# Kernel tuning notes

Measured on AMD Instinct MI355X. Metric: run time of the kernel, lower is better.

Reference implementation:

```python
import jax, jax.numpy as jnp
import numpy as np

NEG_FILL = -10000.0  # matches masked_fill_(mask, -10000.0)


def setup_inputs() -> dict:
    key0 = jax.random.key(0)
    kq, kk, kv, km = jax.random.split(key0, 4)
    B, H, S, D = 2, 16, 2048, 64
    query = jax.random.normal(kq, (B, H, S, D), dtype=jnp.float32)
    key = jax.random.normal(kk, (B, H, S, D), dtype=jnp.float32)
    value = jax.random.normal(kv, (B, H, S, D), dtype=jnp.float32)
    # key-padding mask [B, S]; True = position is masked out
    mask = jax.random.randint(km, (B, S), 0, 2).astype(jnp.bool_)
    return {"query": query, "key": key, "value": value, "mask": mask}


def reference(query, key, value, mask):
    # scaled dot-product attention: [B,H,S,D] x [B,H,S,D] -> [B,H,S,S]
    scale = 1.0 / jnp.sqrt(jnp.asarray(query.shape[-1], query.dtype))
    scores = jnp.einsum('bhqd,bhkd->bhqk', query, key) * scale
    # mask [B,S] -> broadcast over heads and query positions as [B,1,1,S]
    scores = jnp.where(mask[:, None, None, :], jnp.asarray(NEG_FILL, scores.dtype), scores)
    attn = jax.nn.softmax(scores, axis=-1)
    # dropout probs are 0 (eval-mode identity)
    out = jnp.einsum('bhqk,bhkd->bhqd', attn, value)
    return out
```

## Files before the change

### kernel.cpp

```cpp
#include <hip/hip_runtime.h>
#include <hip/hip_bf16.h>
#include <stdint.h>

namespace {

constexpr int Bb = 2;
constexpr int Hh = 16;
constexpr int Ss = 2048;
constexpr int Dd = 64;
constexpr int KT = 64;
constexpr int NT = Ss / KT;
constexpr int TILE_BYTES = KT * Dd * 2;
constexpr int BH_BYTES = NT * TILE_BYTES;
constexpr size_t KPRE_BYTES = (size_t)Bb * Hh * Ss * Dd * 2;
constexpr size_t VPRE_OFF = KPRE_BYTES;
constexpr size_t MASK_OFF = 2 * KPRE_BYTES;
constexpr size_t WS_NEED = MASK_OFF + (size_t)Bb * NT * 8;

typedef __bf16 bf16x8 __attribute__((ext_vector_type(8)));
typedef float floatx4 __attribute__((ext_vector_type(4)));
typedef short short4v __attribute__((ext_vector_type(4)));
typedef short short8v __attribute__((ext_vector_type(8)));

typedef __attribute__((address_space(1))) const unsigned int guint;
typedef __attribute__((address_space(3))) unsigned int luint;

__device__ __forceinline__ void g2lds16(const void* g, void* l) {
  __builtin_amdgcn_global_load_lds((guint*)g, (luint*)l, 16, 0, 0);
}

__device__ __forceinline__ floatx4 mfma16(short4v a, short4v b, floatx4 c) {
#if __has_builtin(__builtin_amdgcn_mfma_f32_16x16x16bf16_1k)
  return __builtin_amdgcn_mfma_f32_16x16x16bf16_1k(a, b, c, 0, 0, 0);
#else
  floatx4 d;
  __asm__("v_mfma_f32_16x16x16_bf16 %0, %1, %2, %3" : "=v"(d) : "v"(a), "v"(b), "v"(c));
  return d;
#endif
}

__device__ __forceinline__ short bf2s(float x) {
  __bf16 h = (__bf16)x;
  return __builtin_bit_cast(short, h);
}

__global__ __launch_bounds__(256) void preprocess(
    const float* __restrict__ K, const float* __restrict__ V,
    const int* __restrict__ mask, uint8_t* __restrict__ ws)
{
  const int t = blockIdx.x * 256 + threadIdx.x;
  if (t < 524288) {
    const int c = t & 7, key = (t >> 3) & 2047, bh = t >> 14;
    const int row = key & 63, tile = key >> 6;
    const float4* src = (const float4*)(K + ((size_t)bh * 2048 + key) * 64 + c * 8);
    const float4 a = src[0], b = src[1];
    bf16x8 pk;
    pk[0] = (__bf16)a.x; pk[1] = (__bf16)a.y; pk[2] = (__bf16)a.z; pk[3] = (__bf16)a.w;
    pk[4] = (__bf16)b.x; pk[5] = (__bf16)b.y; pk[6] = (__bf16)b.z; pk[7] = (__bf16)b.w;
    uint8_t* dst = ws + (size_t)bh * BH_BYTES + tile * TILE_BYTES + row * 128 + ((c ^ (row & 7)) << 4);
    *(bf16x8*)dst = pk;
  } else if (t < 1048576) {
    const int v = t - 524288;
    const int c16 = v & 7, d = (v >> 3) & 63, kt = (v >> 9) & 31, bh = v >> 14;
    const int s2 = c16 & 1, q = c16 >> 1;
    const int kb = kt * 64 + 32 * s2 + q * 4;
    const float* src = V + ((size_t)bh * 2048 + kb) * 64 + d;
    bf16x8 pv;
#pragma unroll
    for (int i = 0; i < 4; ++i) pv[i] = (__bf16)src[i * 64];
#pragma unroll
    for (int i = 0; i < 4; ++i) pv[4 + i] = (__bf16)src[(16 + i) * 64];
    uint8_t* dst = ws + VPRE_OFF + (size_t)bh * BH_BYTES + kt * TILE_BYTES + d * 128 + ((c16 ^ (d & 7)) << 4);
    *(bf16x8*)dst = pv;
  } else if (t < 1048576 + 4096) {
    const int i = t - 1048576;
    const int bb = i >> 11, key = i & 2047;
    const unsigned long long bal = __ballot(mask[bb * 2048 + key] != 0);
    if ((key & 63) == 0)
      ((unsigned long long*)(ws + MASK_OFF))[bb * NT + (key >> 6)] = bal;
  }
}

#define NEGM (-14426.950408889634f)

__global__ __launch_bounds__(256, 2) void attn_fused3(
    const float* __restrict__ Q, const uint8_t* __restrict__ ws,
    float* __restrict__ Out)
{
  const int tid  = threadIdx.x;
  const int wave = tid >> 6;
  const int lane = tid & 63;
  const int ln   = lane & 15;
  const int quad = lane >> 4;

  const int bh   = blockIdx.x;
  const int qblk = blockIdx.y;
  const int b    = bh >> 4;

  const float* Qb = Q + (size_t)bh * Ss * Dd;
  float*       Ob = Out + (size_t)bh * Ss * Dd;
  const uint8_t* Kpre = ws + (size_t)bh * BH_BYTES;
  const uint8_t* Vpre = ws + VPRE_OFF + (size_t)bh * BH_BYTES;
  const unsigned long long* Mbits = (const unsigned long long*)(ws + MASK_OFF) + b * NT;

  __shared__ __align__(16) __bf16 Klds[2][KT * Dd];
  __shared__ __align__(16) __bf16 Vlds[2][KT * Dd];

  const int q0A = qblk * 128 + wave * 32;
  const int q0B = q0A + 16;

  const float QS = 0.125f * 1.44269504088896340736f;
  bf16x8 aqA0, aqA1, aqB0, aqB1;
  {
    const float* qpA = Qb + (size_t)(q0A + ln) * Dd + quad * 8;
    const float* qpB = Qb + (size_t)(q0B + ln) * Dd + quad * 8;
#pragma unroll
    for (int j = 0; j < 8; ++j) {
      aqA0[j] = (__bf16)(qpA[j] * QS);
      aqA1[j] = (__bf16)(qpA[32 + j] * QS);
      aqB0[j] = (__bf16)(qpB[j] * QS);
      aqB1[j] = (__bf16)(qpB[32 + j] * QS);
    }
  }

  floatx4 oA[4], oB[4];
  floatx4 laccA = (floatx4){0.f, 0.f, 0.f, 0.f};
  floatx4 laccB = (floatx4){0.f, 0.f, 0.f, 0.f};
#pragma unroll
  for (int nd = 0; nd < 4; ++nd) {
    oA[nd] = (floatx4){0.f, 0.f, 0.f, 0.f};
    oB[nd] = (floatx4){0.f, 0.f, 0.f, 0.f};
  }

  const int swz0 = (quad ^ (ln & 7)) << 4;
  const int swz1 = ((quad + 4) ^ (ln & 7)) << 4;
  const int soff0 = (wave * 2) * 1024 + lane * 16;
  const int soff1 = soff0 + 1024;

  {
    g2lds16(Kpre + soff0, (uint8_t*)Klds[0] + soff0);
    g2lds16(Vpre + soff0, (uint8_t*)Vlds[0] + soff0);
    g2lds16(Kpre + soff1, (uint8_t*)Klds[0] + soff1);
    g2lds16(Vpre + soff1, (uint8_t*)Vlds[0] + soff1);
  }

  for (int kt = 0; kt < NT; ++kt) {
    const int cur = kt & 1;
    __syncthreads();

    if (kt + 1 < NT) {
      const uint8_t* kg = Kpre + (kt + 1) * TILE_BYTES;
      const uint8_t* vg = Vpre + (kt + 1) * TILE_BYTES;
      uint8_t* kl = (uint8_t*)Klds[cur ^ 1];
      uint8_t* vl = (uint8_t*)Vlds[cur ^ 1];
      g2lds16(kg + soff0, kl + soff0);
      g2lds16(vg + soff0, vl + soff0);
      g2lds16(kg + soff1, kl + soff1);
      g2lds16(vg + soff1, vl + soff1);
    }

    const unsigned long long mb = Mbits[kt];
    const uint32_t mlo = (uint32_t)mb, mhi = (uint32_t)(mb >> 32);

    floatx4 sA[4], sB[4];
#pragma unroll
    for (int t = 0; t < 4; ++t) {
      const uint8_t* krow = (const uint8_t*)Klds[cur] + (t * 16 + ln) * 128;
      const bf16x8 bk0 = *(const bf16x8*)(krow + swz0);
      const bf16x8 bk1 = *(const bf16x8*)(krow + swz1);
      floatx4 cA = (floatx4){0.f, 0.f, 0.f, 0.f};
      cA = __builtin_amdgcn_mfma_f32_16x16x32_bf16(bk0, aqA0, cA, 0, 0, 0);
      cA = __builtin_amdgcn_mfma_f32_16x16x32_bf16(bk1, aqA1, cA, 0, 0, 0);
      sA[t] = cA;
      floatx4 cB = (floatx4){0.f, 0.f, 0.f, 0.f};
      cB = __builtin_amdgcn_mfma_f32_16x16x32_bf16(bk0, aqB0, cB, 0, 0, 0);
      cB = __builtin_amdgcn_mfma_f32_16x16x32_bf16(bk1, aqB1, cB, 0, 0, 0);
      sB[t] = cB;
    }

    short4v bpA[4], bpB[4];
#pragma unroll
    for (int t = 0; t < 4; ++t) {
      const uint32_t bits = ((t & 2) ? mhi : mlo) >> ((t & 1) * 16 + quad * 4);
#pragma unroll
      for (int r = 0; r < 4; ++r) {
        const bool msk = (bits >> r) & 1;
        float pA = __builtin_amdgcn_exp2f(sA[t][r]);
        float pB = __builtin_amdgcn_exp2f(sB[t][r]);
        pA = msk ? 0.f : pA;
        pB = msk ? 0.f : pB;
        laccA[r] += pA;
        laccB[r] += pB;
        bpA[t][r] = bf2s(pA);
        bpB[t][r] = bf2s(pB);
      }
    }

#pragma unroll
    for (int nd = 0; nd < 4; ++nd) {
      const uint8_t* vrow = (const uint8_t*)Vlds[cur] + (nd * 16 + ln) * 128;
#pragma unroll
      for (int s2 = 0; s2 < 2; ++s2) {
        const short8v w = *(const short8v*)(vrow + (((quad * 2 + s2) ^ (ln & 7)) << 4));
        const short4v vlo = __builtin_shufflevector(w, w, 0, 1, 2, 3);
        const short4v vhi = __builtin_shufflevector(w, w, 4, 5, 6, 7);
        oA[nd] = mfma16(vlo, bpA[2 * s2], oA[nd]);
        oA[nd] = mfma16(vhi, bpA[2 * s2 + 1], oA[nd]);
        oB[nd] = mfma16(vlo, bpB[2 * s2], oB[nd]);
        oB[nd] = mfma16(vhi, bpB[2 * s2 + 1], oB[nd]);
      }
    }
  }

  float lA = (laccA[0] + laccA[1]) + (laccA[2] + laccA[3]);
  float lB = (laccB[0] + laccB[1]) + (laccB[2] + laccB[3]);
  lA += __shfl_xor(lA, 16); lA += __shfl_xor(lA, 32);
  lB += __shfl_xor(lB, 16); lB += __shfl_xor(lB, 32);
  const float iA = 1.0f / lA, iB = 1.0f / lB;
#pragma unroll
  for (int nd = 0; nd < 4; ++nd) {
    float4 wv;
    wv.x = oA[nd][0] * iA; wv.y = oA[nd][1] * iA;
    wv.z = oA[nd][2] * iA; wv.w = oA[nd][3] * iA;
    *(float4*)(Ob + (size_t)(q0A + ln) * Dd + nd * 16 + quad * 4) = wv;
    wv.x = oB[nd][0] * iB; wv.y = oB[nd][1] * iB;
    wv.z = oB[nd][2] * iB; wv.w = oB[nd][3] * iB;
    *(float4*)(Ob + (size_t)(q0B + ln) * Dd + nd * 16 + quad * 4) = wv;
  }
}

constexpr int LDK = 72;
__global__ __launch_bounds__(256, 4) void attn_fused(
    const float* __restrict__ Q, const float* __restrict__ K,
    const float* __restrict__ V, const int* __restrict__ mask,
    float* __restrict__ Out)
{
  const int tid  = threadIdx.x;
  const int wave = tid >> 6;
  const int lane = tid & 63;
  const int ln   = lane & 15;
  const int quad = lane >> 4;
  const int qblk = blockIdx.x;
  const int bh   = blockIdx.y;
  const int b    = bh >> 4;

  const float* Qb = Q + (size_t)bh * Ss * Dd;
  const float* Kb = K + (size_t)bh * Ss * Dd;
  const float* Vb = V + (size_t)bh * Ss * Dd;
  float*       Ob = Out + (size_t)bh * Ss * Dd;
  const int*   mrow = mask + b * Ss;

  __shared__ __bf16 Klds[KT * LDK];
  __shared__ __bf16 Vlds[Dd * LDK];
  __shared__ __bf16 Plds[4][16 * LDK];

  const int q0 = qblk * 64 + wave * 16;
  bf16x8 aq0, aq1;
  {
    const float* qp = Qb + (size_t)(q0 + ln) * Dd + quad * 8;
#pragma unroll
    for (int j = 0; j < 8; ++j) aq0[j] = (__bf16)qp[j];
#pragma unroll
    for (int j = 0; j < 8; ++j) aq1[j] = (__bf16)qp[32 + j];
  }
  const float SCALE = 0.125f * 1.44269504088896340736f;
  floatx4 o[4];
  float m_i[4], l_i[4];
#pragma unroll
  for (int nd = 0; nd < 4; ++nd) o[nd] = (floatx4){0.f, 0.f, 0.f, 0.f};
#pragma unroll
  for (int r = 0; r < 4; ++r) { m_i[r] = -INFINITY; l_i[r] = 0.f; }

  for (int kt = 0; kt < NT; ++kt) {
    const int kbase = kt * KT;
    __syncthreads();
#pragma unroll
    for (int i = 0; i < 4; ++i) {
      const int idx = tid + i * 256;
      const int row = idx >> 4;
      const int c4  = (idx & 15) << 2;
      const float4 kv = *(const float4*)(Kb + (size_t)(kbase + row) * Dd + c4);
      __bf16* kd = &Klds[row * LDK + c4];
      kd[0] = (__bf16)kv.x; kd[1] = (__bf16)kv.y;
      kd[2] = (__bf16)kv.z; kd[3] = (__bf16)kv.w;
      const float4 vv = *(const float4*)(Vb + (size_t)(kbase + row) * Dd + c4);
      Vlds[(c4 + 0) * LDK + row] = (__bf16)vv.x;
      Vlds[(c4 + 1) * LDK + row] = (__bf16)vv.y;
      Vlds[(c4 + 2) * LDK + row] = (__bf16)vv.z;
      Vlds[(c4 + 3) * LDK + row] = (__bf16)vv.w;
    }
    __syncthreads();
    floatx4 s[4];
#pragma unroll
    for (int ns = 0; ns < 4; ++ns) {
      const bf16x8 bk0 = *(const bf16x8*)&Klds[(ns * 16 + ln) * LDK + quad * 8];
      const bf16x8 bk1 = *(const bf16x8*)&Klds[(ns * 16 + ln) * LDK + 32 + quad * 8];
      floatx4 c = (floatx4){0.f, 0.f, 0.f, 0.f};
      c = __builtin_amdgcn_mfma_f32_16x16x32_bf16(aq0, bk0, c, 0, 0, 0);
      c = __builtin_amdgcn_mfma_f32_16x16x32_bf16(aq1, bk1, c, 0, 0, 0);
      s[ns] = c;
    }
#pragma unroll
    for (int ns = 0; ns < 4; ++ns) {
      const int msk = mrow[kbase + ns * 16 + ln];
#pragma unroll
      for (int r = 0; r < 4; ++r)
        s[ns][r] = msk ? NEGM : s[ns][r] * SCALE;
    }
    float mt[4];
#pragma unroll
    for (int r = 0; r < 4; ++r) {
      float v0 = fmaxf(fmaxf(s[0][r], s[1][r]), fmaxf(s[2][r], s[3][r]));
      v0 = fmaxf(v0, __shfl_xor(v0, 1));
      v0 = fmaxf(v0, __shfl_xor(v0, 2));
      v0 = fmaxf(v0, __shfl_xor(v0, 4));
      v0 = fmaxf(v0, __shfl_xor(v0, 8));
      mt[r] = v0;
    }
    float alpha[4];
#pragma unroll
    for (int r = 0; r < 4; ++r) {
      const float mnew = fmaxf(m_i[r], mt[r]);
      alpha[r] = __builtin_amdgcn_exp2f(m_i[r] - mnew);
      m_i[r] = mnew;
    }
    float p[4][4];
#pragma unroll
    for (int r = 0; r < 4; ++r) {
      float acc = 0.f;
#pragma unroll
      for (int ns = 0; ns < 4; ++ns) {
        p[ns][r] = __builtin_amdgcn_exp2f(s[ns][r] - m_i[r]);
        acc += p[ns][r];
      }
      acc += __shfl_xor(acc, 1);
      acc += __shfl_xor(acc, 2);
      acc += __shfl_xor(acc, 4);
      acc += __shfl_xor(acc, 8);
      l_i[r] = l_i[r] * alpha[r] + acc;
    }
#pragma unroll
    for (int nd = 0; nd < 4; ++nd)
#pragma unroll
      for (int r = 0; r < 4; ++r) o[nd][r] *= alpha[r];
#pragma unroll
    for (int ns = 0; ns < 4; ++ns)
#pragma unroll
      for (int r = 0; r < 4; ++r)
        Plds[wave][(quad * 4 + r) * LDK + ns * 16 + ln] = (__bf16)p[ns][r];
    __asm__ __volatile__("" ::: "memory");
    const bf16x8 ap0 = *(const bf16x8*)&Plds[wave][ln * LDK + quad * 8];
    const bf16x8 ap1 = *(const bf16x8*)&Plds[wave][ln * LDK + 32 + quad * 8];
#pragma unroll
    for (int nd = 0; nd < 4; ++nd) {
      const bf16x8 bv0 = *(const bf16x8*)&Vlds[(nd * 16 + ln) * LDK + quad * 8];
      const bf16x8 bv1 = *(const bf16x8*)&Vlds[(nd * 16 + ln) * LDK + 32 + quad * 8];
      o[nd] = __builtin_amdgcn_mfma_f32_16x16x32_bf16(ap0, bv0, o[nd], 0, 0, 0);
      o[nd] = __builtin_amdgcn_mfma_f32_16x16x32_bf16(ap1, bv1, o[nd], 0, 0, 0);
    }
  }
#pragma unroll
  for (int r = 0; r < 4; ++r) l_i[r] = 1.0f / l_i[r];
#pragma unroll
  for (int nd = 0; nd < 4; ++nd)
#pragma unroll
    for (int r = 0; r < 4; ++r)
      Ob[(size_t)(q0 + quad * 4 + r) * Dd + nd * 16 + ln] = o[nd][r] * l_i[r];
}

}

extern "C" void kernel_launch(void* const* d_in, const int* in_sizes, int n_in,
                              void* d_out, int out_size, void* d_ws, size_t ws_size,
                              hipStream_t stream) {
  const float* Q   = (const float*)d_in[0];
  const float* K   = (const float*)d_in[1];
  const float* V   = (const float*)d_in[2];
  const int*  mask = (const int*)d_in[3];
  float* Out = (float*)d_out;

  if (ws_size >= WS_NEED) {
    preprocess<<<4112, 256, 0, stream>>>(K, V, mask, (uint8_t*)d_ws);
    attn_fused3<<<dim3(Bb * Hh, Ss / 128), 256, 0, stream>>>(Q, (const uint8_t*)d_ws, Out);
  } else {
    attn_fused<<<dim3(Ss / 64, Bb * Hh), 256, 0, stream>>>(Q, K, V, mask, Out);
  }
}
```

Baseline: 154.0 us.

## Double key tile per iteration and transpose V through LDS in preprocess

The attention kernel now processes 128 keys per loop iteration (two 64-key tiles) with doubled LDS double-buffers. This halves the number of barriers and loop overheads and gives more MFMA work between synchronizations. The preprocess kernel now assigns one block per key tile and transposes V through shared memory with coalesced float4 loads, replacing the strided scalar global reads. The cost is higher LDS use (64KB) and more registers, which may reduce occupancy.

Result: faster. 143.7 us (-6.7%).

```diff
diff --git a/kernel.cpp b/kernel.cpp
--- a/kernel.cpp
+++ b/kernel.cpp
@@ -16,6 +16,8 @@
 constexpr size_t VPRE_OFF = KPRE_BYTES;
 constexpr size_t MASK_OFF = 2 * KPRE_BYTES;
 constexpr size_t WS_NEED = MASK_OFF + (size_t)Bb * NT * 8;
+constexpr int NIT = 16;
+constexpr int IT_BYTES = 2 * TILE_BYTES;
 
 typedef __bf16 bf16x8 __attribute__((ext_vector_type(8)));
 typedef float floatx4 __attribute__((ext_vector_type(4)));
@@ -44,46 +46,68 @@
   return __builtin_bit_cast(short, h);
 }
 
-__global__ __launch_bounds__(256) void preprocess(
+__global__ __launch_bounds__(256) void preprocess2(
     const float* __restrict__ K, const float* __restrict__ V,
     const int* __restrict__ mask, uint8_t* __restrict__ ws)
 {
-  const int t = blockIdx.x * 256 + threadIdx.x;
-  if (t < 524288) {
-    const int c = t & 7, key = (t >> 3) & 2047, bh = t >> 14;
-    const int row = key & 63, tile = key >> 6;
-    const float4* src = (const float4*)(K + ((size_t)bh * 2048 + key) * 64 + c * 8);
-    const float4 a = src[0], b = src[1];
-    bf16x8 pk;
-    pk[0] = (__bf16)a.x; pk[1] = (__bf16)a.y; pk[2] = (__bf16)a.z; pk[3] = (__bf16)a.w;
-    pk[4] = (__bf16)b.x; pk[5] = (__bf16)b.y; pk[6] = (__bf16)b.z; pk[7] = (__bf16)b.w;
-    uint8_t* dst = ws + (size_t)bh * BH_BYTES + tile * TILE_BYTES + row * 128 + ((c ^ (row & 7)) << 4);
-    *(bf16x8*)dst = pk;
-  } else if (t < 1048576) {
-    const int v = t - 524288;
-    const int c16 = v & 7, d = (v >> 3) & 63, kt = (v >> 9) & 31, bh = v >> 14;
-    const int s2 = c16 & 1, q = c16 >> 1;
-    const int kb = kt * 64 + 32 * s2 + q * 4;
-    const float* src = V + ((size_t)bh * 2048 + kb) * 64 + d;
-    bf16x8 pv;
-#pragma unroll
-    for (int i = 0; i < 4; ++i) pv[i] = (__bf16)src[i * 64];
-#pragma unroll
-    for (int i = 0; i < 4; ++i) pv[4 + i] = (__bf16)src[(16 + i) * 64];
-    uint8_t* dst = ws + VPRE_OFF + (size_t)bh * BH_BYTES + kt * TILE_BYTES + d * 128 + ((c16 ^ (d & 7)) << 4);
-    *(bf16x8*)dst = pv;
-  } else if (t < 1048576 + 4096) {
-    const int i = t - 1048576;
+  const int tid = threadIdx.x;
+  const int kt = blockIdx.x;
+  if (blockIdx.y == 32) {
+    if (kt >= 16) return;
+    const int i = kt * 256 + tid;
     const int bb = i >> 11, key = i & 2047;
     const unsigned long long bal = __ballot(mask[bb * 2048 + key] != 0);
     if ((key & 63) == 0)
       ((unsigned long long*)(ws + MASK_OFF))[bb * NT + (key >> 6)] = bal;
+    return;
+  }
+  const int bh = blockIdx.y;
+  __shared__ float Vsh[64 * 68];
+
+  {
+    const int c = tid & 7;
+#pragma unroll
+    for (int half = 0; half < 2; ++half) {
+      const int row = (tid >> 3) + half * 32;
+      const float4* src = (const float4*)(K + ((size_t)bh * 2048 + kt * 64 + row) * 64 + c * 8);
+      const float4 a = src[0], b2 = src[1];
+      bf16x8 pk;
+      pk[0] = (__bf16)a.x;  pk[1] = (__bf16)a.y;  pk[2] = (__bf16)a.z;  pk[3] = (__bf16)a.w;
+      pk[4] = (__bf16)b2.x; pk[5] = (__bf16)b2.y; pk[6] = (__bf16)b2.z; pk[7] = (__bf16)b2.w;
+      uint8_t* dst = ws + (size_t)bh * BH_BYTES + kt * TILE_BYTES + row * 128 + ((c ^ (row & 7)) << 4);
+      *(bf16x8*)dst = pk;
+    }
+  }
+#pragma unroll
+  for (int i = 0; i < 4; ++i) {
+    const int vt = tid + 256 * i;
+    const int row = vt >> 4, c4 = vt & 15;
+    const float4 v4 = *(const float4*)(V + ((size_t)bh * 2048 + kt * 64 + row) * 64 + c4 * 4);
+    *(float4*)&Vsh[row * 68 + c4 * 4] = v4;
+  }
+  __syncthreads();
+  {
+    const int c16 = tid & 7;
+    const int s2 = c16 & 1, q = c16 >> 1;
+    const int k0 = 32 * s2 + 4 * q;
+#pragma unroll
+    for (int half = 0; half < 2; ++half) {
+      const int d = (tid >> 3) + half * 32;
+      bf16x8 pv;
+#pragma unroll
+      for (int j = 0; j < 4; ++j) {
+        pv[j]     = (__bf16)Vsh[(k0 + j) * 68 + d];
+        pv[4 + j] = (__bf16)Vsh[(k0 + 16 + j) * 68 + d];
+      }
+      uint8_t* dst = ws + VPRE_OFF + (size_t)bh * BH_BYTES + kt * TILE_BYTES + d * 128 + ((c16 ^ (d & 7)) << 4);
+      *(bf16x8*)dst = pv;
+    }
   }
 }
 
 #define NEGM (-14426.950408889634f)
 
-__global__ __launch_bounds__(256, 2) void attn_fused3(
+__global__ __launch_bounds__(256, 2) void attn_fused4(
     const float* __restrict__ Q, const uint8_t* __restrict__ ws,
     float* __restrict__ Out)
 {
@@ -103,8 +127,8 @@
   const uint8_t* Vpre = ws + VPRE_OFF + (size_t)bh * BH_BYTES;
   const unsigned long long* Mbits = (const unsigned long long*)(ws + MASK_OFF) + b * NT;
 
-  __shared__ __align__(16) __bf16 Klds[2][KT * Dd];
-  __shared__ __align__(16) __bf16 Vlds[2][KT * Dd];
+  __shared__ __align__(16) __bf16 Klds[2][128 * Dd];
+  __shared__ __align__(16) __bf16 Vlds[2][128 * Dd];
 
   const int q0A = qblk * 128 + wave * 32;
   const int q0B = q0A + 16;
@@ -134,80 +158,84 @@
 
   const int swz0 = (quad ^ (ln & 7)) << 4;
   const int swz1 = ((quad + 4) ^ (ln & 7)) << 4;
-  const int soff0 = (wave * 2) * 1024 + lane * 16;
-  const int soff1 = soff0 + 1024;
-
-  {
-    g2lds16(Kpre + soff0, (uint8_t*)Klds[0] + soff0);
-    g2lds16(Vpre + soff0, (uint8_t*)Vlds[0] + soff0);
-    g2lds16(Kpre + soff1, (uint8_t*)Klds[0] + soff1);
-    g2lds16(Vpre + soff1, (uint8_t*)Vlds[0] + soff1);
-  }
-
-  for (int kt = 0; kt < NT; ++kt) {
-    const int cur = kt & 1;
+  const int soff = wave * 4096 + lane * 16;
+
+#pragma unroll
+  for (int i = 0; i < 4; ++i) {
+    g2lds16(Kpre + soff + i * 1024, (uint8_t*)Klds[0] + soff + i * 1024);
+    g2lds16(Vpre + soff + i * 1024, (uint8_t*)Vlds[0] + soff + i * 1024);
+  }
+
+  for (int kt2 = 0; kt2 < NIT; ++kt2) {
+    const int cur = kt2 & 1;
     __syncthreads();
 
-    if (kt + 1 < NT) {
-      const uint8_t* kg = Kpre + (kt + 1) * TILE_BYTES;
-      const uint8_t* vg = Vpre + (kt + 1) * TILE_BYTES;
+    if (kt2 + 1 < NIT) {
+      const uint8_t* kg = Kpre + (kt2 + 1) * IT_BYTES;
+      const uint8_t* vg = Vpre + (kt2 + 1) * IT_BYTES;
       uint8_t* kl = (uint8_t*)Klds[cur ^ 1];
       uint8_t* vl = (uint8_t*)Vlds[cur ^ 1];
-      g2lds16(kg + soff0, kl + soff0);
-      g2lds16(vg + soff0, vl + soff0);
-      g2lds16(kg + soff1, kl + soff1);
-      g2lds16(vg + soff1, vl + soff1);
-    }
-
-    const unsigned long long mb = Mbits[kt];
-    const uint32_t mlo = (uint32_t)mb, mhi = (uint32_t)(mb >> 32);
-
-    floatx4 sA[4], sB[4];
-#pragma unroll
-    for (int t = 0; t < 4; ++t) {
-      const uint8_t* krow = (const uint8_t*)Klds[cur] + (t * 16 + ln) * 128;
+#pragma unroll
+      for (int i = 0; i < 4; ++i) {
+        g2lds16(kg + soff + i * 1024, kl + soff + i * 1024);
+        g2lds16(vg + soff + i * 1024, vl + soff + i * 1024);
+      }
+    }
+
+    const unsigned long long mb0 = Mbits[2 * kt2];
+    const unsigned long long mb1 = Mbits[2 * kt2 + 1];
+
+    floatx4 sA[8], sB[8];
+#pragma unroll
+    for (int sub = 0; sub < 8; ++sub) {
+      const uint8_t* krow = (const uint8_t*)Klds[cur] + (sub >> 2) * 8192 + ((sub & 3) * 16 + ln) * 128;
       const bf16x8 bk0 = *(const bf16x8*)(krow + swz0);
       const bf16x8 bk1 = *(const bf16x8*)(krow + swz1);
       floatx4 cA = (floatx4){0.f, 0.f, 0.f, 0.f};
       cA = __builtin_amdgcn_mfma_f32_16x16x32_bf16(bk0, aqA0, cA, 0, 0, 0);
       cA = __builtin_amdgcn_mfma_f32_16x16x32_bf16(bk1, aqA1, cA, 0, 0, 0);
-      sA[t] = cA;
+      sA[sub] = cA;
       floatx4 cB = (floatx4){0.f, 0.f, 0.f, 0.f};
       cB = __builtin_amdgcn_mfma_f32_16x16x32_bf16(bk0, aqB0, cB, 0, 0, 0);
       cB = __builtin_amdgcn_mfma_f32_16x16x32_bf16(bk1, aqB1, cB, 0, 0, 0);
-      sB[t] = cB;
-    }
-
-    short4v bpA[4], bpB[4];
-#pragma unroll
-    for (int t = 0; t < 4; ++t) {
-      const uint32_t bits = ((t & 2) ? mhi : mlo) >> ((t & 1) * 16 + quad * 4);
+      sB[sub] = cB;
+    }
+
+    short4v bpA[8], bpB[8];
+#pragma unroll
+    for (int sub = 0; sub < 8; ++sub) {
+      const unsigned long long mbx = (sub & 4) ? mb1 : mb0;
+      const uint32_t bits = (uint32_t)(mbx >> ((sub & 3) * 16 + quad * 4));
 #pragma unroll
       for (int r = 0; r < 4; ++r) {
         const bool msk = (bits >> r) & 1;
-        float pA = __builtin_amdgcn_exp2f(sA[t][r]);
-        float pB = __builtin_amdgcn_exp2f(sB[t][r]);
+        float pA = __builtin_amdgcn_exp2f(sA[sub][r]);
+        float pB = __builtin_amdgcn_exp2f(sB[sub][r]);
         pA = msk ? 0.f : pA;
         pB = msk ? 0.f : pB;
         laccA[r] += pA;
         laccB[r] += pB;
-        bpA[t][r] = bf2s(pA);
-        bpB[t][r] = bf2s(pB);
+        bpA[sub][r] = bf2s(pA);
+        bpB[sub][r] = bf2s(pB);
       }
     }
 
 #pragma unroll
     for (int nd = 0; nd < 4; ++nd) {
-      const uint8_t* vrow = (const uint8_t*)Vlds[cur] + (nd * 16 + ln) * 128;
-#pragma unroll
-      for (int s2 = 0; s2 < 2; ++s2) {
-        const short8v w = *(const short8v*)(vrow + (((quad * 2 + s2) ^ (ln & 7)) << 4));
-        const short4v vlo = __builtin_shufflevector(w, w, 0, 1, 2, 3);
-        const short4v vhi = __builtin_shufflevector(w, w, 4, 5, 6, 7);
-        oA[nd] = mfma16(vlo, bpA[2 * s2], oA[nd]);
-        oA[nd] = mfma16(vhi, bpA[2 * s2 + 1], oA[nd]);
-        oB[nd] = mfma16(vlo, bpB[2 * s2], oB[nd]);
-        oB[nd] = mfma16(vhi, bpB[2 * s2 + 1], oB[nd]);
+#pragma unroll
+      for (int T = 0; T < 2; ++T) {
+        const uint8_t* vrow = (const uint8_t*)Vlds[cur] + T * 8192 + (nd * 16 + ln) * 128;
+#pragma unroll
+        for (int s2 = 0; s2 < 2; ++s2) {
+          const short8v w = *(const short8v*)(vrow + (((quad * 2 + s2) ^ (ln & 7)) << 4));
+          const short4v vlo = __builtin_shufflevector(w, w, 0, 1, 2, 3);
+          const short4v vhi = __builtin_shufflevector(w, w, 4, 5, 6, 7);
+          const int sub0 = T * 4 + 2 * s2;
+          oA[nd] = mfma16(vlo, bpA[sub0], oA[nd]);
+          oA[nd] = mfma16(vhi, bpA[sub0 + 1], oA[nd]);
+          oB[nd] = mfma16(vlo, bpB[sub0], oB[nd]);
+          oB[nd] = mfma16(vhi, bpB[sub0 + 1], oB[nd]);
+        }
       }
     }
   }
@@ -380,8 +408,8 @@
   float* Out = (float*)d_out;
 
   if (ws_size >= WS_NEED) {
-    preprocess<<<4112, 256, 0, stream>>>(K, V, mask, (uint8_t*)d_ws);
-    attn_fused3<<<dim3(Bb * Hh, Ss / 128), 256, 0, stream>>>(Q, (const uint8_t*)d_ws, Out);
+    preprocess2<<<dim3(32, 33), 256, 0, stream>>>(K, V, mask, (uint8_t*)d_ws);
+    attn_fused4<<<dim3(Bb * Hh, Ss / 128), 256, 0, stream>>>(Q, (const uint8_t*)d_ws, Out);
   } else {
     attn_fused<<<dim3(Ss / 64, Bb * Hh), 256, 0, stream>>>(Q, K, V, mask, Out);
   }
```
